# Kernel tuning notes

Measured on AMD Instinct MI355X. Metric: run time of the kernel, lower is better.

Reference implementation:

```python
import jax, jax.numpy as jnp
import numpy as np

N = 768                       # atoms
E = N * (N - 1)               # complete directed graph edges
DIM = 64                      # hidden dim
CUT = 5.0                     # rbf high
NC = 50                       # n_centers = ceil(5/0.1)
ODIM = 1                      # output_dim
NCONV = 3
_centers_np = np.linspace(0.0, CUT, NC)
CENTERS = jnp.asarray(_centers_np, jnp.float32)
GAP = float(_centers_np[1] - _centers_np[0])
RO_IN = 2 * ODIM + NC         # readout input: 2*output_dim + rbf fan_out = 52


def softplus_bt(x, beta, thr):
    # torch.nn.Softplus(beta, threshold): linear above threshold
    bx = beta * x
    return jnp.where(bx > thr, x, jax.nn.softplus(bx) / beta)


def rbf(d):
    # exp(-(1/gap) * (d - mu_k)^2); d: (..., 1) -> (..., NC)
    return jnp.exp((-1.0 / GAP) * (d - CENTERS) ** 2)


def setup_inputs() -> dict:
    key = jax.random.key(0)
    ks = jax.random.split(key, 24)
    atom_types = jax.random.randint(ks[0], (N,), 0, 100)
    edge_distances = jax.random.uniform(ks[1], (E, 1), jnp.float32) * CUT
    # complete directed graph, edge order matches the nested i,j loop (i!=j)
    ii = np.repeat(np.arange(N), N)
    jj = np.tile(np.arange(N), N)
    m = ii != jj
    src = jnp.asarray(ii[m], jnp.int32)
    dst = jnp.asarray(jj[m], jnp.int32)

    def p(k, shape, fan):
        return jax.random.normal(k, shape, jnp.float32) / np.sqrt(fan)

    embedding = p(ks[2], (100, DIM), DIM).at[0].set(0.0)  # padding_idx=0
    L = NCONV
    return {
        'atom_types': atom_types, 'edge_distances': edge_distances,
        'src': src, 'dst': dst, 'embedding': embedding,
        'w1': p(ks[3], (L, DIM, DIM), DIM),                 # node_layer1 (no bias)
        'pw1': p(ks[4], (L, NC, DIM), NC), 'pb1': p(ks[5], (L, DIM), NC),
        'pw2': p(ks[6], (L, DIM, DIM), DIM), 'pb2': p(ks[7], (L, DIM), DIM),
        'qw1': p(ks[8], (L, DIM, DIM), DIM), 'qb1': p(ks[9], (L, DIM), DIM),
        'qw2': p(ks[10], (L, DIM, DIM), DIM), 'qb2': p(ks[11], (L, DIM), DIM),
        'au_w1': p(ks[12], (DIM, 64), DIM), 'au_b1': p(ks[13], (64,), DIM),
        'au_w2': p(ks[14], (64, ODIM), 64), 'au_b2': p(ks[15], (ODIM,), 64),
        'ro_w1': p(ks[16], (RO_IN, 64), RO_IN), 'ro_b1': p(ks[17], (64,), RO_IN),
        'ro_w2': p(ks[18], (64, 2), 64), 'ro_b2': p(ks[19], (2,), 64),
    }


def reference(atom_types, edge_distances, src, dst, embedding,
              w1, pw1, pb1, pw2, pb2, qw1, qb1, qw2, qb2,
              au_w1, au_b1, au_w2, au_b2, ro_w1, ro_b1, ro_w2, ro_b2):
    h = embedding[atom_types]                       # (N, DIM)
    rbf_out = rbf(edge_distances)                   # (E, NC)
    for l in range(NCONV):
        nw = h @ w1[l]                              # node weights (N, DIM)
        e = softplus_bt(rbf_out @ pw1[l] + pb1[l], 0.5, 14) @ pw2[l] + pb2[l]  # (E, DIM)
        msg = nw[src] * e                           # gather-mul (E, DIM)
        agg = jax.ops.segment_sum(msg, dst, num_segments=N)  # scatter-sum (N, DIM)
        upd = softplus_bt(agg @ qw1[l] + qb1[l], 0.5, 14) @ qw2[l] + qb2[l]
        h = h + upd
    # atom_update with ShiftSoftplus (beta=1, shift=2, threshold=20)
    ha = softplus_bt(h @ au_w1 + au_b1, 1.0, 20) - jnp.log(jnp.float32(2.0))
    ha = ha @ au_w2 + au_b2                         # (N, ODIM)
    # readout over all ordered pairs i!=j, in edge order == (src, dst)
    edge_feat = jnp.concatenate([ha[src], ha[dst], rbf_out], axis=-1)  # (E, 52)
    logits = jax.nn.relu(edge_feat @ ro_w1 + ro_b1) @ ro_w2 + ro_b2    # (E, 2)
    return jax.nn.softmax(logits, axis=-1)
```

## Files before the change

### kernel.cpp

```cpp
#include <hip/hip_runtime.h>
#include <hip/hip_fp16.h>

#define NATOMS 768
#define NM1    767
#define NEDGE  (768*767)
#define DIM    64
#define NC     50
#define GAPF   (5.0f/49.0f)
#define NIGAP  (-49.0f/5.0f)
#define G      512
#define STEPF  (5.0f/511.0f)
#define INVSTEP (511.0f/5.0f)
#define G2      256
#define STEPC   (5.0f/255.0f)
#define INVSTEPC (255.0f/5.0f)
#define LN2F   0.693147180559945f

#define WS_H     0
#define WS_NWA   49152
#define WS_NWB   73728
#define WS_HA    98304
#define WS_DISTT 99328
#define WS_TTC   689152
#define WS_TTR   738304

__device__ __forceinline__ float softplus05(float x) {
    float bx = 0.5f * x;
    return (bx > 14.0f) ? x : 2.0f * __logf(1.0f + __expf(bx));
}
__device__ __forceinline__ int lane_bcast_i(int v, int l) {
    return __builtin_amdgcn_readlane(v, l);
}
__device__ __forceinline__ float lane_bcast_f(float v, int l) {
    return __uint_as_float((unsigned)__builtin_amdgcn_readlane((int)__float_as_uint(v), l));
}
__device__ __forceinline__ float2 pair2f(unsigned p) {
    __half2 h = *reinterpret_cast<__half2*>(&p);
    return __half22float2(h);
}

__global__ __launch_bounds__(256)
void k_pre(const int* __restrict__ types, const float* __restrict__ dist,
           const float* __restrict__ emb, const float* __restrict__ w1all,
           const float* __restrict__ pw1, const float* __restrict__ pb1,
           const float* __restrict__ pw2, const float* __restrict__ pb2,
           const float* __restrict__ row1, const float* __restrict__ rob1,
           float* __restrict__ ws) {
    __shared__ float s_t[4 * 64];
    __shared__ float s_tile[64][65];
    const int tid = threadIdx.x, widx = tid >> 6, c = tid & 63;
    float*  h     = ws + WS_H;
    __half* nwh   = (__half*)(ws + WS_NWA);
    float*  distT = ws + WS_DISTT;
    __half* TTCh  = (__half*)(ws + WS_TTC);
    __half* TTRh  = (__half*)(ws + WS_TTR);
    const int b = blockIdx.x;

    if (b < 192) {
        const int w = b * 4 + widx, tbl = w >> 8, g = w & 255;
        const float d = g * STEPC;
        const float* W1 = pw1 + tbl * NC * DIM;
        float t1 = pb1[tbl * DIM + c];
        for (int k = 0; k < NC; ++k) {
            float x = d - GAPF * (float)k;
            t1 = fmaf(__expf(NIGAP * x * x), W1[k * DIM + c], t1);
        }
        s_t[widx * 64 + c] = softplus05(t1);
        const float* W2 = pw2 + tbl * DIM * DIM;
        float val = pb2[tbl * DIM + c];
        #pragma unroll 8
        for (int k = 0; k < DIM; ++k)
            val = fmaf(s_t[widx * 64 + k], W2[k * DIM + c], val);
        __half* TTt = TTCh + tbl * (G2 * DIM * 2);
        TTt[(g * DIM + c) * 2] = __float2half(val);
        if (g > 0) TTt[((g - 1) * DIM + c) * 2 + 1] = __float2half(val);
    } else if (b < 320) {
        const int g = (b - 192) * 4 + widx;
        const float d = g * STEPF;
        float val = rob1[c];
        for (int k = 0; k < NC; ++k) {
            float x = d - GAPF * (float)k;
            val = fmaf(__expf(NIGAP * x * x), row1[(2 + k) * DIM + c], val);
        }
        TTRh[(g * DIM + c) * 2] = __float2half(val);
        if (g > 0) TTRh[((g - 1) * DIM + c) * 2 + 1] = __float2half(val);
    } else if (b < 512) {
        const int i = (b - 320) * 4 + widx;
        float hv = emb[types[i] * DIM + c];
        h[i * DIM + c] = hv;
        s_t[widx * 64 + c] = hv;
        float acc = 0.0f;
        #pragma unroll 8
        for (int k = 0; k < DIM; ++k)
            acc = fmaf(s_t[widx * 64 + k], w1all[k * DIM + c], acc);
        nwh[(i >> 1) * 128 + c * 2 + (i & 1)] = __float2half(acc);
    } else {
        const int t = b - 512;
        const int I0 = (t / 12) * 64, J0 = (t % 12) * 64;
        #pragma unroll 4
        for (int r = 0; r < 16; ++r) {
            const int i = I0 + widx * 16 + r;
            const int j = J0 + c;
            s_tile[widx * 16 + r][c] =
                (i == j) ? 0.0f : dist[i * NM1 + (j - (j > i))];
        }
        __syncthreads();
        #pragma unroll 4
        for (int r = 0; r < 16; ++r) {
            const int j = J0 + widx * 16 + r;
            const int i = I0 + c;
            distT[j * NATOMS + i] = s_tile[c][widx * 16 + r];
        }
    }
}

__global__ __launch_bounds__(512)
void k_edgeupd(const __half2* __restrict__ TTl, const float* __restrict__ distT,
               const __half2* __restrict__ nwin,
               const float* __restrict__ qw1, const float* __restrict__ qb1,
               const float* __restrict__ qw2, const float* __restrict__ qb2,
               float* __restrict__ h,
               const float* __restrict__ wnext, __half* __restrict__ nwout,
               const float* __restrict__ auw1, const float* __restrict__ aub1,
               const float* __restrict__ auw2, const float* __restrict__ aub2,
               float* __restrict__ ha, int last) {
    __shared__ float s_part[8][64];
    __shared__ float s_upd[192];
    const int tid = threadIdx.x, widx = tid >> 6, c = tid & 63;
    const int j = blockIdx.x;
    const int s0 = widx * 96;

    const char* TTb = (const char*)TTl + c * 4;
    float csum = 0.0f;
    {
        float d = distT[j * NATOMS + s0 + c];
        float pos = d * INVSTEPC;
        int g = (int)pos;
        g = (g < 0) ? 0 : ((g > 254) ? 254 : g);
        float f = pos - (float)g;
        int kx = g * 256;
        const char* nwrow = (const char*)(nwin + (s0 >> 1) * 64 + c);
        for (int grp = 0; grp < 4; ++grp) {
            unsigned sa[8], sb[8], sn[8];
            #pragma unroll
            for (int u = 0; u < 8; ++u) {
                const int t = grp * 8 + u;
                int kx0 = lane_bcast_i(kx, 2 * t);
                int kx1 = lane_bcast_i(kx, 2 * t + 1);
                sa[u] = *(const unsigned*)(TTb + kx0);
                sb[u] = *(const unsigned*)(TTb + kx1);
                sn[u] = __builtin_nontemporal_load((const unsigned*)(nwrow + t * 256));
            }
            #pragma unroll
            for (int u = 0; u < 8; ++u) {
                const int t = grp * 8 + u;
                float f0 = lane_bcast_f(f, 2 * t);
                float f1 = lane_bcast_f(f, 2 * t + 1);
                float2 ta = pair2f(sa[u]);
                float2 tb = pair2f(sb[u]);
                float2 nwf = pair2f(sn[u]);
                float e0 = fmaf(f0, ta.y - ta.x, ta.x);
                float e1 = fmaf(f1, tb.y - tb.x, tb.x);
                csum = fmaf(e0, nwf.x, csum);
                csum = fmaf(e1, nwf.y, csum);
            }
        }
    }
    {
        float d = distT[j * NATOMS + s0 + 64 + (c & 31)];
        float pos = d * INVSTEPC;
        int g = (int)pos;
        g = (g < 0) ? 0 : ((g > 254) ? 254 : g);
        float f = pos - (float)g;
        int kx = g * 256;
        const char* nwrow = (const char*)(nwin + ((s0 + 64) >> 1) * 64 + c);
        for (int grp = 0; grp < 2; ++grp) {
            unsigned sa[8], sb[8], sn[8];
            #pragma unroll
            for (int u = 0; u < 8; ++u) {
                const int t = grp * 8 + u;
                int kx0 = lane_bcast_i(kx, 2 * t);
                int kx1 = lane_bcast_i(kx, 2 * t + 1);
                sa[u] = *(const unsigned*)(TTb + kx0);
                sb[u] = *(const unsigned*)(TTb + kx1);
                sn[u] = __builtin_nontemporal_load((const unsigned*)(nwrow + t * 256));
            }
            #pragma unroll
            for (int u = 0; u < 8; ++u) {
                const int t = grp * 8 + u;
                float f0 = lane_bcast_f(f, 2 * t);
                float f1 = lane_bcast_f(f, 2 * t + 1);
                float2 ta = pair2f(sa[u]);
                float2 tb = pair2f(sb[u]);
                float2 nwf = pair2f(sn[u]);
                float e0 = fmaf(f0, ta.y - ta.x, ta.x);
                float e1 = fmaf(f1, tb.y - tb.x, tb.x);
                csum = fmaf(e0, nwf.x, csum);
                csum = fmaf(e1, nwf.y, csum);
            }
        }
    }
    s_part[widx][c] = csum;
    __syncthreads();

    if (widx == 0) {
        float tot = 0.0f;
        #pragma unroll
        for (int w8 = 0; w8 < 8; ++w8) tot += s_part[w8][c];
        float2 t0 = __half22float2(*(const __half2*)TTb);
        float nwj = __half2float(((const __half*)nwin)[(j >> 1) * 128 + c * 2 + (j & 1)]);
        tot -= t0.x * nwj;
        s_upd[c] = tot;
        float t = qb1[c];
        #pragma unroll 8
        for (int k = 0; k < DIM; ++k) t = fmaf(s_upd[k], qw1[k * DIM + c], t);
        s_upd[64 + c] = softplus05(t);
        float o = qb2[c];
        #pragma unroll 8
        for (int k = 0; k < DIM; ++k) o = fmaf(s_upd[64 + k], qw2[k * DIM + c], o);
        float hn = h[j * DIM + c] + o;
        h[j * DIM + c] = hn;
        s_upd[128 + c] = hn;
        if (!last) {
            float v = 0.0f;
            #pragma unroll 8
            for (int k = 0; k < DIM; ++k) v = fmaf(s_upd[128 + k], wnext[k * DIM + c], v);
            nwout[(j >> 1) * 128 + c * 2 + (j & 1)] = __float2half(v);
        } else {
            float t2 = aub1[c];
            #pragma unroll 8
            for (int k = 0; k < DIM; ++k) t2 = fmaf(s_upd[128 + k], auw1[k * DIM + c], t2);
            t2 = ((t2 > 20.0f) ? t2 : __logf(1.0f + __expf(t2))) - LN2F;
            float v = t2 * auw2[c];
            #pragma unroll
            for (int s = 32; s > 0; s >>= 1) v += __shfl_down(v, s, 64);
            if (c == 0) ha[j] = v + aub2[0];
        }
    }
}

__global__ __launch_bounds__(256)
void k_ro(const float* __restrict__ dist, const float* __restrict__ ha,
          const __half2* __restrict__ TTro,
          const float* __restrict__ row1, const float* __restrict__ row2,
          const float* __restrict__ rob2, float* __restrict__ out) {
    __shared__ float s_h[4][16 * 65];
    __shared__ float s_w2[128];
    const int tid = threadIdx.x, widx = tid >> 6, c = tid & 63;
    if (tid < 128) s_w2[tid] = row2[tid];
    __syncthreads();
    const int ebase = (blockIdx.x * 4 + widx) * 64;

    int kxv; float ff, fa, fb;
    {
        int eg = ebase + c;
        float d = dist[eg];
        float pos = d * INVSTEP;
        int kk = (int)pos;
        kk = (kk < 0) ? 0 : ((kk > 510) ? 510 : kk);
        kxv = kk * 256;
        ff = pos - (float)kk;
        unsigned i = (unsigned)(((unsigned long long)(unsigned)eg * 2867044662ull) >> 41);
        int r = eg - (int)i * 767;
        int jd = r + (r >= (int)i);
        fa = ha[i];
        fb = ha[jd];
    }
    const char* TTb2 = (const char*)TTro + c * 4;
    const float wa = row1[c], wb = row1[DIM + c];
    const int e2 = (c >> 1) & 15, p2 = c & 1, kh = c >> 5;
    const float bias2 = (kh == 0) ? rob2[p2] : 0.0f;
    float* sh = s_h[widx];
    #pragma unroll
    for (int ch = 0; ch < 4; ++ch) {
        #pragma unroll
        for (int half = 0; half < 2; ++half) {
            unsigned st[8];
            #pragma unroll
            for (int u = 0; u < 8; ++u) {
                const int le = ch * 16 + half * 8 + u;
                int kxu = lane_bcast_i(kxv, le);
                st[u] = *(const unsigned*)(TTb2 + kxu);
            }
            #pragma unroll
            for (int u = 0; u < 8; ++u) {
                const int le = ch * 16 + half * 8 + u;
                const int e = half * 8 + u;
                float fu  = lane_bcast_f(ff, le);
                float fau = lane_bcast_f(fa, le);
                float fbu = lane_bcast_f(fb, le);
                float2 tt = pair2f(st[u]);
                float hv = fmaf(fu, tt.y - tt.x, tt.x);
                hv = fmaf(fau, wa, hv);
                hv = fmaf(fbu, wb, hv);
                sh[e * 65 + c] = fmaxf(hv, 0.0f);
            }
        }
        float lsum = bias2;
        #pragma unroll 8
        for (int k8 = 0; k8 < 32; ++k8) {
            int k = kh * 32 + k8;
            lsum = fmaf(sh[e2 * 65 + k], s_w2[2 * k + p2], lsum);
        }
        lsum += __shfl_xor(lsum, 32, 64);
        float other = __shfl_xor(lsum, 1, 64);
        float m = fmaxf(lsum, other);
        float ea = __expf(lsum - m), eb = __expf(other - m);
        float r = ea / (ea + eb);
        if (c < 32) out[ebase * 2 + ch * 32 + c] = r;
    }
}

extern "C" void kernel_launch(void* const* d_in, const int* in_sizes, int n_in,
                              void* d_out, int out_size, void* d_ws, size_t ws_size,
                              hipStream_t stream) {
    const int*   types = (const int*)d_in[0];
    const float* dist  = (const float*)d_in[1];
    const float* emb   = (const float*)d_in[4];
    const float* w1    = (const float*)d_in[5];
    const float* pw1   = (const float*)d_in[6];
    const float* pb1   = (const float*)d_in[7];
    const float* pw2   = (const float*)d_in[8];
    const float* pb2   = (const float*)d_in[9];
    const float* qw1   = (const float*)d_in[10];
    const float* qb1   = (const float*)d_in[11];
    const float* qw2   = (const float*)d_in[12];
    const float* qb2   = (const float*)d_in[13];
    const float* auw1  = (const float*)d_in[14];
    const float* aub1  = (const float*)d_in[15];
    const float* auw2  = (const float*)d_in[16];
    const float* aub2  = (const float*)d_in[17];
    const float* row1  = (const float*)d_in[18];
    const float* rob1  = (const float*)d_in[19];
    const float* row2  = (const float*)d_in[20];
    const float* rob2  = (const float*)d_in[21];

    float* ws   = (float*)d_ws;
    float* outp = (float*)d_out;
    const __half2* TTC = (const __half2*)(ws + WS_TTC);
    const __half2* TTR = (const __half2*)(ws + WS_TTR);
    __half2* nwbuf[2] = { (__half2*)(ws + WS_NWA), (__half2*)(ws + WS_NWB) };

    k_pre<<<656, 256, 0, stream>>>(types, dist, emb, w1, pw1, pb1, pw2, pb2,
                                   row1, rob1, ws);
    for (int l = 0; l < 3; ++l) {
        k_edgeupd<<<768, 512, 0, stream>>>(TTC + l * (G2 * DIM),
            ws + WS_DISTT, nwbuf[l & 1],
            qw1 + l * DIM * DIM, qb1 + l * DIM,
            qw2 + l * DIM * DIM, qb2 + l * DIM,
            ws + WS_H,
            (l < 2) ? (w1 + (l + 1) * DIM * DIM) : w1, (__half*)nwbuf[(l + 1) & 1],
            auw1, aub1, auw2, aub2, ws + WS_HA, (l == 2) ? 1 : 0);
    }
    k_ro<<<2301, 256, 0, stream>>>(dist, ws + WS_HA, TTR,
                                   row1, row2, rob2, outp);
}
```

Measured before the change: 186.5 us.

## Stage per-layer filter table in LDS and de-interleave table and node-weight layouts

New measurement: 201.2 us. 1.08x slower.

```diff
diff --git a/kernel.cpp b/kernel.cpp
--- a/kernel.cpp
+++ b/kernel.cpp
@@ -22,7 +22,7 @@
 #define WS_HA    98304
 #define WS_DISTT 99328
 #define WS_TTC   689152
-#define WS_TTR   738304
+#define WS_TTR   713728
 
 __device__ __forceinline__ float softplus05(float x) {
     float bx = 0.5f * x;
@@ -71,9 +71,7 @@
         #pragma unroll 8
         for (int k = 0; k < DIM; ++k)
             val = fmaf(s_t[widx * 64 + k], W2[k * DIM + c], val);
-        __half* TTt = TTCh + tbl * (G2 * DIM * 2);
-        TTt[(g * DIM + c) * 2] = __float2half(val);
-        if (g > 0) TTt[((g - 1) * DIM + c) * 2 + 1] = __float2half(val);
+        TTCh[tbl * (G2 * DIM) + g * DIM + c] = __float2half(val);
     } else if (b < 320) {
         const int g = (b - 192) * 4 + widx;
         const float d = g * STEPF;
@@ -93,7 +91,7 @@
         #pragma unroll 8
         for (int k = 0; k < DIM; ++k)
             acc = fmaf(s_t[widx * 64 + k], w1all[k * DIM + c], acc);
-        nwh[(i >> 1) * 128 + c * 2 + (i & 1)] = __float2half(acc);
+        nwh[i * 64 + c] = __float2half(acc);
     } else {
         const int t = b - 512;
         const int I0 = (t / 12) * 64, J0 = (t % 12) * 64;
@@ -114,9 +112,9 @@
     }
 }
 
-__global__ __launch_bounds__(512)
-void k_edgeupd(const __half2* __restrict__ TTl, const float* __restrict__ distT,
-               const __half2* __restrict__ nwin,
+__global__ __launch_bounds__(512, 8)
+void k_edgeupd(const __half* __restrict__ TTl, const float* __restrict__ distT,
+               const __half* __restrict__ nwin,
                const float* __restrict__ qw1, const float* __restrict__ qb1,
                const float* __restrict__ qw2, const float* __restrict__ qb2,
                float* __restrict__ h,
@@ -124,92 +122,87 @@
                const float* __restrict__ auw1, const float* __restrict__ aub1,
                const float* __restrict__ auw2, const float* __restrict__ aub2,
                float* __restrict__ ha, int last) {
+    __shared__ unsigned s_tab[G2 * 32];
     __shared__ float s_part[8][64];
     __shared__ float s_upd[192];
     const int tid = threadIdx.x, widx = tid >> 6, c = tid & 63;
     const int j = blockIdx.x;
     const int s0 = widx * 96;
-
-    const char* TTb = (const char*)TTl + c * 4;
-    float csum = 0.0f;
+    const int half = c >> 5, cl = c & 31;
+
     {
-        float d = distT[j * NATOMS + s0 + c];
-        float pos = d * INVSTEPC;
+        const uint4* src = (const uint4*)TTl;
+        uint4* dst = (uint4*)s_tab;
+        #pragma unroll
+        for (int it = 0; it < 4; ++it)
+            dst[tid + it * 512] = src[tid + it * 512];
+    }
+    __syncthreads();
+
+    const unsigned* tabl = s_tab + cl;
+    const char* nwb = (const char*)nwin + half * 128 + cl * 4;
+    float2 csum = make_float2(0.0f, 0.0f);
+    {
+        float pos = distT[j * NATOMS + s0 + c] * INVSTEPC;
         int g = (int)pos;
         g = (g < 0) ? 0 : ((g > 254) ? 254 : g);
         float f = pos - (float)g;
-        int kx = g * 256;
-        const char* nwrow = (const char*)(nwin + (s0 >> 1) * 64 + c);
-        for (int grp = 0; grp < 4; ++grp) {
-            unsigned sa[8], sb[8], sn[8];
-            #pragma unroll
-            for (int u = 0; u < 8; ++u) {
-                const int t = grp * 8 + u;
-                int kx0 = lane_bcast_i(kx, 2 * t);
-                int kx1 = lane_bcast_i(kx, 2 * t + 1);
-                sa[u] = *(const unsigned*)(TTb + kx0);
-                sb[u] = *(const unsigned*)(TTb + kx1);
-                sn[u] = __builtin_nontemporal_load((const unsigned*)(nwrow + t * 256));
-            }
-            #pragma unroll
-            for (int u = 0; u < 8; ++u) {
-                const int t = grp * 8 + u;
-                float f0 = lane_bcast_f(f, 2 * t);
-                float f1 = lane_bcast_f(f, 2 * t + 1);
-                float2 ta = pair2f(sa[u]);
-                float2 tb = pair2f(sb[u]);
-                float2 nwf = pair2f(sn[u]);
-                float e0 = fmaf(f0, ta.y - ta.x, ta.x);
-                float e1 = fmaf(f1, tb.y - tb.x, tb.x);
-                csum = fmaf(e0, nwf.x, csum);
-                csum = fmaf(e1, nwf.y, csum);
-            }
+        int kw = g * 32;
+        const char* nwrow = nwb + s0 * 128;
+        #pragma unroll 8
+        for (int t = 0; t < 32; ++t) {
+            int kw0 = lane_bcast_i(kw, 2 * t);
+            int kw1 = lane_bcast_i(kw, 2 * t + 1);
+            float f0 = lane_bcast_f(f, 2 * t);
+            float f1 = lane_bcast_f(f, 2 * t + 1);
+            int kws = half ? kw1 : kw0;
+            float fs = half ? f1 : f0;
+            float2 lo = pair2f(tabl[kws]);
+            float2 hi = pair2f(tabl[kws + 32]);
+            float2 nwf = pair2f(*(const unsigned*)(nwrow + t * 256));
+            float e0 = fmaf(fs, hi.x - lo.x, lo.x);
+            float e1 = fmaf(fs, hi.y - lo.y, lo.y);
+            csum.x = fmaf(e0, nwf.x, csum.x);
+            csum.y = fmaf(e1, nwf.y, csum.y);
         }
     }
     {
-        float d = distT[j * NATOMS + s0 + 64 + (c & 31)];
-        float pos = d * INVSTEPC;
+        float pos = distT[j * NATOMS + s0 + 64 + cl] * INVSTEPC;
         int g = (int)pos;
         g = (g < 0) ? 0 : ((g > 254) ? 254 : g);
         float f = pos - (float)g;
-        int kx = g * 256;
-        const char* nwrow = (const char*)(nwin + ((s0 + 64) >> 1) * 64 + c);
-        for (int grp = 0; grp < 2; ++grp) {
-            unsigned sa[8], sb[8], sn[8];
-            #pragma unroll
-            for (int u = 0; u < 8; ++u) {
-                const int t = grp * 8 + u;
-                int kx0 = lane_bcast_i(kx, 2 * t);
-                int kx1 = lane_bcast_i(kx, 2 * t + 1);
-                sa[u] = *(const unsigned*)(TTb + kx0);
-                sb[u] = *(const unsigned*)(TTb + kx1);
-                sn[u] = __builtin_nontemporal_load((const unsigned*)(nwrow + t * 256));
-            }
-            #pragma unroll
-            for (int u = 0; u < 8; ++u) {
-                const int t = grp * 8 + u;
-                float f0 = lane_bcast_f(f, 2 * t);
-                float f1 = lane_bcast_f(f, 2 * t + 1);
-                float2 ta = pair2f(sa[u]);
-                float2 tb = pair2f(sb[u]);
-                float2 nwf = pair2f(sn[u]);
-                float e0 = fmaf(f0, ta.y - ta.x, ta.x);
-                float e1 = fmaf(f1, tb.y - tb.x, tb.x);
-                csum = fmaf(e0, nwf.x, csum);
-                csum = fmaf(e1, nwf.y, csum);
-            }
-        }
-    }
-    s_part[widx][c] = csum;
+        int kw = g * 32;
+        const char* nwrow = nwb + (s0 + 64) * 128;
+        #pragma unroll 8
+        for (int t = 0; t < 16; ++t) {
+            int kw0 = lane_bcast_i(kw, 2 * t);
+            int kw1 = lane_bcast_i(kw, 2 * t + 1);
+            float f0 = lane_bcast_f(f, 2 * t);
+            float f1 = lane_bcast_f(f, 2 * t + 1);
+            int kws = half ? kw1 : kw0;
+            float fs = half ? f1 : f0;
+            float2 lo = pair2f(tabl[kws]);
+            float2 hi = pair2f(tabl[kws + 32]);
+            float2 nwf = pair2f(*(const unsigned*)(nwrow + t * 256));
+            float e0 = fmaf(fs, hi.x - lo.x, lo.x);
+            float e1 = fmaf(fs, hi.y - lo.y, lo.y);
+            csum.x = fmaf(e0, nwf.x, csum.x);
+            csum.y = fmaf(e1, nwf.y, csum.y);
+        }
+    }
+    float2 tot2;
+    tot2.x = csum.x + __shfl_xor(csum.x, 32, 64);
+    tot2.y = csum.y + __shfl_xor(csum.y, 32, 64);
+    if (half == 0) *(float2*)&s_part[widx][2 * cl] = tot2;
     __syncthreads();
 
     if (widx == 0) {
         float tot = 0.0f;
         #pragma unroll
         for (int w8 = 0; w8 < 8; ++w8) tot += s_part[w8][c];
-        float2 t0 = __half22float2(*(const __half2*)TTb);
-        float nwj = __half2float(((const __half*)nwin)[(j >> 1) * 128 + c * 2 + (j & 1)]);
-        tot -= t0.x * nwj;
+        float t0 = __half2float(((const __half*)s_tab)[c]);
+        float nwj = __half2float(nwin[j * 64 + c]);
+        tot -= t0 * nwj;
         s_upd[c] = tot;
         float t = qb1[c];
         #pragma unroll 8
@@ -225,7 +218,7 @@
             float v = 0.0f;
             #pragma unroll 8
             for (int k = 0; k < DIM; ++k) v = fmaf(s_upd[128 + k], wnext[k * DIM + c], v);
-            nwout[(j >> 1) * 128 + c * 2 + (j & 1)] = __float2half(v);
+            nwout[j * 64 + c] = __float2half(v);
         } else {
             float t2 = aub1[c];
             #pragma unroll 8
@@ -337,9 +330,9 @@
 
     float* ws   = (float*)d_ws;
     float* outp = (float*)d_out;
-    const __half2* TTC = (const __half2*)(ws + WS_TTC);
+    const __half*  TTC = (const __half*)(ws + WS_TTC);
     const __half2* TTR = (const __half2*)(ws + WS_TTR);
-    __half2* nwbuf[2] = { (__half2*)(ws + WS_NWA), (__half2*)(ws + WS_NWB) };
+    __half* nwbuf[2] = { (__half*)(ws + WS_NWA), (__half*)(ws + WS_NWB) };
 
     k_pre<<<656, 256, 0, stream>>>(types, dist, emb, w1, pw1, pb1, pw2, pb2,
                                    row1, rob1, ws);
@@ -349,7 +342,7 @@
             qw1 + l * DIM * DIM, qb1 + l * DIM,
             qw2 + l * DIM * DIM, qb2 + l * DIM,
             ws + WS_H,
-            (l < 2) ? (w1 + (l + 1) * DIM * DIM) : w1, (__half*)nwbuf[(l + 1) & 1],
+            (l < 2) ? (w1 + (l + 1) * DIM * DIM) : w1, nwbuf[(l + 1) & 1],
             auw1, aub1, auw2, aub2, ws + WS_HA, (l == 2) ? 1 : 0);
     }
     k_ro<<<2301, 256, 0, stream>>>(dist, ws + WS_HA, TTR,
```
